# Kernel tuning notes

Measured on AMD Instinct MI355X. Metric: run time of the kernel, lower is better.

Reference implementation:

```python
import jax, jax.numpy as jnp
import numpy as np

N = 50000      # nodes
E = 1600000    # edges (avg degree 32)
D = 128        # feature dim (hardcoded by GATConv(128,128,1))
K = 3          # propagation order
NEG_SLOPE = 0.2  # DGL GATConv default leaky_relu slope


def setup_inputs() -> dict:
    key = jax.random.key(0)
    k1, k2, k3, k4, k5, k6, k7 = jax.random.split(key, 7)
    feats = jax.random.normal(k1, (N, D), dtype=jnp.float32)
    src = jax.random.randint(k2, (E,), 0, N, dtype=jnp.int32)
    dst = jax.random.randint(k3, (E,), 0, N, dtype=jnp.int32)
    W = jax.random.normal(k4, (D, D), dtype=jnp.float32) * 0.05
    attn_l = jax.random.normal(k5, (D,), dtype=jnp.float32) * 0.05
    attn_r = jax.random.normal(k6, (D,), dtype=jnp.float32) * 0.05
    bias = jax.random.normal(k7, (D,), dtype=jnp.float32) * 0.05
    return {"feats": feats, "W": W, "attn_l": attn_l, "attn_r": attn_r,
            "bias": bias, "src": src, "dst": dst}


def _grand_conv(feats, src, dst, order):
    seg = jax.ops.segment_sum
    ones = jnp.ones((src.shape[0],), feats.dtype)
    deg_in = jnp.maximum(seg(ones, dst, num_segments=N), 1.0)
    deg_out = jnp.maximum(seg(ones, src, num_segments=N), 1.0)
    norm1 = deg_in ** -0.5   # dst-side (in-degree) norm
    norm2 = deg_out ** -0.5  # src-side (out-degree) norm
    # rst = D_in^-1/2 A D_out^-1/2 feats  (one SpMM)
    nf = feats * norm2[:, None]
    rst = seg(nf[src], dst, num_segments=N) * norm1[:, None]
    # edge weight = norm1[src] * norm2[dst]  (fn.u_mul_v)
    w = (norm1[src] * norm2[dst])[:, None]  # [E,1]
    x = rst
    y = feats  # note: rst itself is NOT added (faithful to source)
    for _ in range(order):
        x = seg(x[src] * w, dst, num_segments=N)  # SpMM hop
        y = y + x
    return y / (order + 1)


def _gat(feat, W, attn_l, attn_r, bias, src, dst):
    seg = jax.ops.segment_sum
    h = feat @ W                      # [N,D]
    el = h @ attn_l                   # [N]
    er = h @ attn_r                   # [N]
    e = jax.nn.leaky_relu(el[src] + er[dst], NEG_SLOPE)  # [E]
    m = jax.ops.segment_max(e, dst, num_segments=N)      # stable edge-softmax
    a = jnp.exp(e - m[dst])
    s = seg(a, dst, num_segments=N)
    alpha = a / s[dst]
    out = seg(h[src] * alpha[:, None], dst, num_segments=N)
    return jax.nn.relu(out + bias)


def reference(feats, W, attn_l, attn_r, bias, src, dst):
    # drop_node with rate 0.0 is identity; S=1 so stacked mean is identity too.
    feat = _grand_conv(feats, src, dst, K)
    logits = _gat(feat, W, attn_l, attn_r, bias, src, dst)
    return jax.nn.log_softmax(logits, axis=-1)
```

## Files before the change

kernel.cpp:

```cpp
#include <hip/hip_runtime.h>
#include <hip/hip_bf16.h>
#include <math.h>

#define D 128
#define SB 512
#define GNUM 256
#define MAXW4 12512

typedef __attribute__((ext_vector_type(8))) short bf16x8;
typedef __attribute__((ext_vector_type(4))) float f32x4;
typedef __attribute__((ext_vector_type(2))) float fv2;

__device__ __forceinline__ bf16x8 pack8(const float* r) {
    union { bf16x8 v; __hip_bfloat162 h[4]; } u;
#pragma unroll
    for (int i = 0; i < 4; ++i)
        u.h[i] = __float22bfloat162_rn(make_float2(r[2 * i], r[2 * i + 1]));
    return u.v;
}

__device__ __forceinline__ uint2 packfp8x8(const float* r) {
    unsigned int w0 = 0, w1 = 0;
    w0 = __builtin_amdgcn_cvt_pk_fp8_f32(r[0], r[1], w0, false);
    w0 = __builtin_amdgcn_cvt_pk_fp8_f32(r[2], r[3], w0, true);
    w1 = __builtin_amdgcn_cvt_pk_fp8_f32(r[4], r[5], w1, false);
    w1 = __builtin_amdgcn_cvt_pk_fp8_f32(r[6], r[7], w1, true);
    return make_uint2(w0, w1);
}

__device__ __forceinline__ float fast_exp2(float x) {
#if __has_builtin(__builtin_amdgcn_exp2f)
    return __builtin_amdgcn_exp2f(x);
#else
    return exp2f(x);
#endif
}

__global__ __launch_bounds__(256) void histo_both(const int* __restrict__ src,
                                                  const int* __restrict__ dst,
                                                  unsigned int* __restrict__ Hs,
                                                  unsigned int* __restrict__ Hd,
                                                  int E, int N) {
    __shared__ unsigned int h[2 * MAXW4];
    int words = (N + 3) >> 2;
    for (int i = threadIdx.x; i < 2 * words; i += 256) h[i] = 0;
    __syncthreads();
    int per = (E + GNUM - 1) / GNUM;
    int lo = blockIdx.x * per;
    int hi = min(E, lo + per);
    for (int e = lo + (int)threadIdx.x; e < hi; e += 256) {
        int s = src[e];
        int d = dst[e];
        atomicAdd(&h[s >> 2], 1u << ((s & 3) * 8));
        atomicAdd(&h[words + (d >> 2)], 1u << ((d & 3) * 8));
    }
    __syncthreads();
    unsigned int* hsrow = Hs + (size_t)blockIdx.x * words;
    unsigned int* hdrow = Hd + (size_t)blockIdx.x * words;
    for (int i = threadIdx.x; i < words; i += 256) {
        hsrow[i] = h[i];
        hdrow[i] = h[words + i];
    }
}

__global__ void col_sum8(const unsigned char* __restrict__ H, float* __restrict__ n2, int N) {
    int bin = blockIdx.x * blockDim.x + threadIdx.x;
    if (bin >= N) return;
    size_t stride = (size_t)(((N + 3) >> 2) * 4);
    unsigned int s = 0;
    for (int b = 0; b < GNUM; ++b) s += H[(size_t)b * stride + bin];
    n2[bin] = rsqrtf((float)max((int)s, 1));
}

__global__ void col_scan8(unsigned char* __restrict__ Hd, int* __restrict__ deg_in,
                          float* __restrict__ n1, int N) {
    int bin = blockIdx.x * blockDim.x + threadIdx.x;
    if (bin >= N) return;
    size_t stride = (size_t)(((N + 3) >> 2) * 4);
    unsigned int run = 0;
    for (int b = 0; b < GNUM; ++b) {
        size_t o = (size_t)b * stride + bin;
        unsigned int hv = Hd[o];
        Hd[o] = (unsigned char)run;
        run += hv;
    }
    deg_in[bin] = (int)run;
    n1[bin] = rsqrtf((float)max((int)run, 1));
}

__global__ void scan_blocks(const int* __restrict__ in, int* __restrict__ out,
                            int* __restrict__ sums, int n) {
    __shared__ int sh[SB];
    int gid = blockIdx.x * SB + threadIdx.x;
    int v = (gid < n) ? in[gid] : 0;
    sh[threadIdx.x] = v;
    __syncthreads();
    for (int off = 1; off < SB; off <<= 1) {
        int t = (threadIdx.x >= off) ? sh[threadIdx.x - off] : 0;
        __syncthreads();
        sh[threadIdx.x] += t;
        __syncthreads();
    }
    if (gid < n) out[gid] = sh[threadIdx.x] - v;
    if (threadIdx.x == SB - 1) sums[blockIdx.x] = sh[threadIdx.x];
}

__global__ void scan_sums(int* sums, int nb) {
    __shared__ int sh[SB];
    int v = (threadIdx.x < nb) ? sums[threadIdx.x] : 0;
    sh[threadIdx.x] = v;
    __syncthreads();
    for (int off = 1; off < SB; off <<= 1) {
        int t = (threadIdx.x >= off) ? sh[threadIdx.x - off] : 0;
        __syncthreads();
        sh[threadIdx.x] += t;
        __syncthreads();
    }
    if (threadIdx.x < nb) sums[threadIdx.x] = sh[threadIdx.x] - v;
}

__global__ void scan_add(int* out, const int* __restrict__ sums, int n, int E) {
    int gid = blockIdx.x * SB + threadIdx.x;
    if (gid < n) out[gid] += sums[blockIdx.x];
    if (blockIdx.x == 0 && threadIdx.x == 0) out[n] = E;
}

__global__ __launch_bounds__(256) void fill_part(const int* __restrict__ src,
                                                 const int* __restrict__ dst,
                                                 const int* __restrict__ rowp,
                                                 const unsigned char* __restrict__ base,
                                                 int* __restrict__ csr, int E, int N) {
    __shared__ unsigned int cur[MAXW4];
    int words = (N + 3) >> 2;
    for (int i = threadIdx.x; i < words; i += 256) cur[i] = 0;
    __syncthreads();
    size_t stride = (size_t)(words * 4);
    int per = (E + GNUM - 1) / GNUM;
    int lo = blockIdx.x * per;
    int hi = min(E, lo + per);
    const unsigned char* brow = base + (size_t)blockIdx.x * stride;
    for (int e = lo + (int)threadIdx.x; e < hi; e += 256) {
        int d = dst[e];
        unsigned int sh = (d & 3) * 8;
        unsigned int r = atomicAdd(&cur[d >> 2], 1u << sh);
        int rank = (int)((r >> sh) & 0xFFu);
        int pos = rowp[d] + (int)brow[d] + rank;
        csr[pos] = src[e];
    }
}

__global__ void convert_nf8(const float* __restrict__ feats, const float* __restrict__ n2,
                            unsigned int* __restrict__ nf8, int N) {
    int t = blockIdx.x * blockDim.x + threadIdx.x;
    int n = t >> 5, l = t & 31;
    if (n >= N) return;
    float w = n2[n];
    float4 f = *reinterpret_cast<const float4*>(feats + (size_t)n * D + l * 4);
    unsigned int w0 = 0;
    w0 = __builtin_amdgcn_cvt_pk_fp8_f32(f.x * w, f.y * w, w0, false);
    w0 = __builtin_amdgcn_cvt_pk_fp8_f32(f.z * w, f.w * w, w0, true);
    nf8[(size_t)n * 32 + l] = w0;
}

__global__ void convert_W(const float* __restrict__ W, ushort* __restrict__ Wb) {
    int tid = blockIdx.x * blockDim.x + threadIdx.x;
    if (tid >= 2048) return;
    int c = tid >> 8, t = (tid >> 6) & 3, lane = tid & 63;
    int col = c * 16 + (lane & 15);
    int k0 = t * 32 + ((lane >> 4) << 3);
    ushort* outp = Wb + (size_t)tid * 8;
    for (int j = 0; j < 8; ++j) {
        __hip_bfloat16 b = __float2bfloat16(W[(size_t)(k0 + j) * D + col]);
        outp[j] = *reinterpret_cast<ushort*>(&b);
    }
}

template <int MODE>
__global__ __launch_bounds__(256) void spmm4(const uint2* __restrict__ xs8,
                                             const ushort* __restrict__ ypin,
                                             const float* __restrict__ feats,
                                             const int* __restrict__ rowp,
                                             const int* __restrict__ csr,
                                             const float* __restrict__ n1,
                                             const float* __restrict__ n2,
                                             ushort* __restrict__ yp,
                                             uint2* __restrict__ outs8, int N) {
    int lane = threadIdx.x & 63;
    int g = lane >> 4, c = lane & 15;
    int wid = ((blockIdx.x * blockDim.x + threadIdx.x) >> 6) * 4 + g;
    if (wid >= N) return;
    int beg = rowp[wid], end = rowp[wid + 1];
    fv2 acc2[4] = {{0.f, 0.f}, {0.f, 0.f}, {0.f, 0.f}, {0.f, 0.f}};
    for (int base = beg; base < end; base += 8) {
        int rem = end - base;
        int kn = rem < 8 ? rem : 8;
        int s_c = csr[base + min(c & 7, rem - 1)];
        uint2 v[8];
#pragma unroll
        for (int k = 0; k < 8; ++k) {
            int sk = __shfl(s_c, k, 16);
            if (k < kn) v[k] = xs8[(size_t)sk * 16 + c];
        }
#pragma unroll
        for (int k = 0; k < 8; ++k)
            if (k < kn) {
                acc2[0] += __builtin_amdgcn_cvt_pk_f32_fp8(v[k].x, false);
                acc2[1] += __builtin_amdgcn_cvt_pk_f32_fp8(v[k].x, true);
                acc2[2] += __builtin_amdgcn_cvt_pk_f32_fp8(v[k].y, false);
                acc2[3] += __builtin_amdgcn_cvt_pk_f32_fp8(v[k].y, true);
            }
    }
    float acc[8];
#pragma unroll
    for (int j = 0; j < 4; ++j) {
        acc[2 * j] = acc2[j][0];
        acc[2 * j + 1] = acc2[j][1];
    }
    if (MODE == 0) {
        float s1 = n1[wid];
        float sc = s1 * s1;
        float r[8];
#pragma unroll
        for (int i = 0; i < 8; ++i) r[i] = acc[i] * sc;
        outs8[(size_t)wid * 16 + c] = packfp8x8(r);
    } else if (MODE == 1 || MODE == 2) {
        float sp = n2[wid];
        float ss = sp * n1[wid];
        float xv[8], rs[8];
#pragma unroll
        for (int i = 0; i < 8; ++i) { xv[i] = acc[i] * sp; rs[i] = acc[i] * ss; }
        if (MODE == 2) {
            bf16x8 prev = *reinterpret_cast<const bf16x8*>(ypin + (size_t)wid * 128 + c * 8);
            const __hip_bfloat162* h2 = reinterpret_cast<const __hip_bfloat162*>(&prev);
#pragma unroll
            for (int i = 0; i < 4; ++i) {
                float2 v = __bfloat1622float2(h2[i]);
                xv[2 * i] += v.x;
                xv[2 * i + 1] += v.y;
            }
        }
        *reinterpret_cast<bf16x8*>(yp + (size_t)wid * 128 + c * 8) = pack8(xv);
        outs8[(size_t)wid * 16 + c] = packfp8x8(rs);
    } else {
        float sp = n2[wid];
        float4 f0 = *reinterpret_cast<const float4*>(feats + (size_t)wid * D + c * 8);
        float4 f1 = *reinterpret_cast<const float4*>(feats + (size_t)wid * D + c * 8 + 4);
        float ft[8] = {f0.x, f0.y, f0.z, f0.w, f1.x, f1.y, f1.z, f1.w};
        bf16x8 prev = *reinterpret_cast<const bf16x8*>(ypin + (size_t)wid * 128 + c * 8);
        const __hip_bfloat162* h2 = reinterpret_cast<const __hip_bfloat162*>(&prev);
        float r[8];
#pragma unroll
        for (int i = 0; i < 4; ++i) {
            float2 v = __bfloat1622float2(h2[i]);
            r[2 * i]     = 0.25f * (ft[2 * i] + v.x + acc[2 * i] * sp);
            r[2 * i + 1] = 0.25f * (ft[2 * i + 1] + v.y + acc[2 * i + 1] * sp);
        }
        *reinterpret_cast<bf16x8*>(yp + (size_t)wid * 128 + c * 8) = pack8(r);
    }
}

__global__ __launch_bounds__(256) void gat4(const uint2* __restrict__ h8,
                                            const int* __restrict__ rowp,
                                            const int* __restrict__ csr,
                                            const float2* __restrict__ elsc,
                                            const float* __restrict__ er,
                                            const float* __restrict__ bias,
                                            float* __restrict__ out, int N) {
    int lane = threadIdx.x & 63;
    int g = lane >> 4, c = lane & 15;
    int wid = ((blockIdx.x * blockDim.x + threadIdx.x) >> 6) * 4 + g;
    if (wid >= N) return;
    int beg = rowp[wid], end = rowp[wid + 1];
    float ern = er[wid];
    float ssum = 0.f;
    fv2 acc2[4] = {{0.f, 0.f}, {0.f, 0.f}, {0.f, 0.f}, {0.f, 0.f}};
    for (int base = beg; base < end; base += 8) {
        int rem = end - base;
        int kn = rem < 8 ? rem : 8;
        int s_c = csr[base + min(c & 7, rem - 1)];
        uint2 v[8];
        float2 es[8];
#pragma unroll
        for (int k = 0; k < 8; ++k) {
            int sk = __shfl(s_c, k, 16);
            if (k < kn) {
                v[k] = h8[(size_t)sk * 16 + c];
                es[k] = elsc[sk];
            }
        }
#pragma unroll
        for (int k = 0; k < 8; ++k)
            if (k < kn) {
                float t = es[k].x + ern;
                t = fmaxf(t, 0.2f * t);
                float p = fast_exp2(t);
                ssum += p;
                float w = p * es[k].y;
                fv2 wv = {w, w};
                acc2[0] += wv * __builtin_amdgcn_cvt_pk_f32_fp8(v[k].x, false);
                acc2[1] += wv * __builtin_amdgcn_cvt_pk_f32_fp8(v[k].x, true);
                acc2[2] += wv * __builtin_amdgcn_cvt_pk_f32_fp8(v[k].y, false);
                acc2[3] += wv * __builtin_amdgcn_cvt_pk_f32_fp8(v[k].y, true);
            }
    }
    float inv = ssum > 0.f ? 1.f / ssum : 0.f;
    float z[8];
    float mx = -INFINITY;
#pragma unroll
    for (int i = 0; i < 8; ++i) {
        z[i] = fmaxf(acc2[i >> 1][i & 1] * inv + bias[16 * i + c], 0.f);
        mx = fmaxf(mx, z[i]);
    }
#pragma unroll
    for (int off = 1; off < 16; off <<= 1) mx = fmaxf(mx, __shfl_xor(mx, off));
    float pz = 0.f;
#pragma unroll
    for (int i = 0; i < 8; ++i) pz += __expf(z[i] - mx);
#pragma unroll
    for (int off = 1; off < 16; off <<= 1) pz += __shfl_xor(pz, off);
    float ls = logf(pz);
    float* op = out + (size_t)wid * D;
#pragma unroll
    for (int i = 0; i < 8; ++i) op[16 * i + c] = z[i] - mx - ls;
}

__global__ __launch_bounds__(256) void gemm_mfma(const ushort* __restrict__ ybf,
                                                 const ushort* __restrict__ Wb,
                                                 const float* __restrict__ attnl,
                                                 const float* __restrict__ attnr,
                                                 unsigned char* __restrict__ h8,
                                                 float2* __restrict__ elsc,
                                                 float* __restrict__ er, int N) {
    __shared__ ushort Ws[16384];
    {
        const float4* srcv = reinterpret_cast<const float4*>(Wb);
        float4* dstv = reinterpret_cast<float4*>(Ws);
        for (int i = threadIdx.x; i < 2048; i += 256) dstv[i] = srcv[i];
    }
    __syncthreads();
    int wave = threadIdx.x >> 6, lane = threadIdx.x & 63;
    int base = blockIdx.x * 64 + wave * 16;
    if (base >= N) return;
    int col16 = lane & 15, rgrp = lane >> 4;

    int arow = base + col16;
    const bf16x8* yrow = reinterpret_cast<const bf16x8*>(ybf + (size_t)arow * 128);
    bf16x8 afrag[4];
#pragma unroll
    for (int t = 0; t < 4; ++t) afrag[t] = yrow[t * 4 + rgrp];

    const bf16x8* WsV = reinterpret_cast<const bf16x8*>(Ws);
    f32x4 acc[8];
#pragma unroll
    for (int c = 0; c < 8; ++c) acc[c] = (f32x4){0.f, 0.f, 0.f, 0.f};
#pragma unroll
    for (int c = 0; c < 8; ++c) {
#pragma unroll
        for (int t = 0; t < 4; ++t) {
            bf16x8 b = WsV[(c * 4 + t) * 64 + lane];
            acc[c] = __builtin_amdgcn_mfma_f32_16x16x32_bf16(afrag[t], b, acc[c], 0, 0, 0);
        }
    }

    float pl[4] = {0.f, 0.f, 0.f, 0.f}, pr[4] = {0.f, 0.f, 0.f, 0.f};
#pragma unroll
    for (int c = 0; c < 8; ++c) {
        float alc = attnl[c * 16 + col16];
        float arc = attnr[c * 16 + col16];
#pragma unroll
        for (int r = 0; r < 4; ++r) {
            pl[r] += acc[c][r] * alc;
            pr[r] += acc[c][r] * arc;
        }
    }
#pragma unroll
    for (int r = 0; r < 4; ++r) {
#pragma unroll
        for (int off = 8; off; off >>= 1) {
            pl[r] += __shfl_xor(pl[r], off);
            pr[r] += __shfl_xor(pr[r], off);
        }
    }

    float rmax[4];
#pragma unroll
    for (int r = 0; r < 4; ++r) {
        float m = 0.f;
#pragma unroll
        for (int c = 0; c < 8; ++c) m = fmaxf(m, fabsf(acc[c][r]));
#pragma unroll
        for (int off = 1; off < 16; off <<= 1) m = fmaxf(m, __shfl_xor(m, off));
        rmax[r] = fmaxf(m, 1e-20f);
    }

#pragma unroll
    for (int r = 0; r < 4; ++r) {
        float iv = 448.f / rmax[r];
        float rr[8];
#pragma unroll
        for (int c = 0; c < 8; ++c) rr[c] = acc[c][r] * iv;
        uint2 pk = packfp8x8(rr);
        int row = base + rgrp * 4 + r;
        *reinterpret_cast<uint2*>(h8 + (size_t)row * 128 + col16 * 8) = pk;
    }

    const float LOG2E = 1.44269504088896340736f;
    if (col16 == 0) {
#pragma unroll
        for (int r = 0; r < 4; ++r) {
            int row = base + rgrp * 4 + r;
            elsc[row] = make_float2(pl[r] * LOG2E, rmax[r] * (1.f / 448.f));
            er[row] = pr[r] * LOG2E;
        }
    }
}

extern "C" void kernel_launch(void* const* d_in, const int* in_sizes, int n_in,
                              void* d_out, int out_size, void* d_ws, size_t ws_size,
                              hipStream_t stream) {
    const float* feats  = (const float*)d_in[0];
    const float* W      = (const float*)d_in[1];
    const float* attn_l = (const float*)d_in[2];
    const float* attn_r = (const float*)d_in[3];
    const float* bias   = (const float*)d_in[4];
    const int*   src    = (const int*)d_in[5];
    const int*   dst    = (const int*)d_in[6];
    int N = in_sizes[0] / D;
    int E = in_sizes[5];
    float* out = (float*)d_out;

    char* p = (char*)d_ws;
    auto alloc = [&](size_t bytes) {
        char* r = p;
        p += (bytes + 255) & ~size_t(255);
        return r;
    };
    int*    deg_in = (int*)alloc((size_t)N * 4);
    int*    rowp   = (int*)alloc(((size_t)N + 1) * 4);
    int*    bsums  = (int*)alloc((size_t)SB * 4);
    float*  n1     = (float*)alloc((size_t)N * 4);
    float*  n2     = (float*)alloc((size_t)N * 4);
    float*  er     = (float*)alloc((size_t)N * 4);
    float2* elsc   = (float2*)alloc((size_t)N * 8);
    int*    csr    = (int*)alloc((size_t)E * 4);
    ushort* Wb     = (ushort*)alloc((size_t)16384 * 2);
    ushort* bufY1  = (ushort*)alloc((size_t)N * 128 * 2);
    ushort* bufY   = (ushort*)alloc((size_t)N * 128 * 2);
    uint2*  t0     = (uint2*)alloc((size_t)N * 16 * 8);
    uint2*  t1     = (uint2*)alloc((size_t)N * 16 * 8);
    uint2*  t2     = (uint2*)alloc((size_t)N * 16 * 8);
    unsigned int* Hs = (unsigned int*)bufY1;
    unsigned int* Hd = (unsigned int*)bufY;

    const int tb = 256;
    histo_both<<<GNUM, tb, 0, stream>>>(src, dst, Hs, Hd, E, N);
    col_sum8<<<(N + tb - 1) / tb, tb, 0, stream>>>((const unsigned char*)Hs, n2, N);
    col_scan8<<<(N + tb - 1) / tb, tb, 0, stream>>>((unsigned char*)Hd, deg_in, n1, N);
    int nb = (N + SB - 1) / SB;
    scan_blocks<<<nb, SB, 0, stream>>>(deg_in, rowp, bsums, N);
    scan_sums<<<1, SB, 0, stream>>>(bsums, nb);
    scan_add<<<nb, SB, 0, stream>>>(rowp, bsums, N, E);
    fill_part<<<GNUM, tb, 0, stream>>>(src, dst, rowp, (const unsigned char*)Hd, csr, E, N);
    convert_W<<<8, tb, 0, stream>>>(W, Wb);
    convert_nf8<<<((size_t)N * 32 + tb - 1) / tb, tb, 0, stream>>>(feats, n2,
                                                                   (unsigned int*)t1, N);

    int wgrid4 = (N + 15) / 16;
    spmm4<0><<<wgrid4, 256, 0, stream>>>(t1, nullptr, nullptr, rowp, csr, n1, n2,
                                         nullptr, t0, N);
    spmm4<1><<<wgrid4, 256, 0, stream>>>(t0, nullptr, nullptr, rowp, csr, n1, n2,
                                         bufY1, t1, N);
    spmm4<2><<<wgrid4, 256, 0, stream>>>(t1, bufY1, nullptr, rowp, csr, n1, n2,
                                         bufY1, t2, N);
    spmm4<3><<<wgrid4, 256, 0, stream>>>(t2, bufY1, feats, rowp, csr, n1, n2,
                                         bufY, nullptr, N);

    gemm_mfma<<<(N + 63) / 64, 256, 0, stream>>>(bufY, Wb, attn_l, attn_r,
                                                 (unsigned char*)t0, elsc, er, N);
    gat4<<<wgrid4, 256, 0, stream>>>((const uint2*)t0, rowp, csr, elsc, er, bias, out, N);
}
```

Baseline: 264.5 us.

## Use 8-lane 16-byte gathers per row in SpMM and GAT kernels

```diff
diff --git a/kernel.cpp b/kernel.cpp
--- a/kernel.cpp
+++ b/kernel.cpp
@@ -26,6 +26,51 @@
     w1 = __builtin_amdgcn_cvt_pk_fp8_f32(r[4], r[5], w1, false);
     w1 = __builtin_amdgcn_cvt_pk_fp8_f32(r[6], r[7], w1, true);
     return make_uint2(w0, w1);
+}
+
+__device__ __forceinline__ uint4 packfp8x16(const float* r) {
+    uint4 o;
+    unsigned int w;
+    w = 0;
+    w = __builtin_amdgcn_cvt_pk_fp8_f32(r[0], r[1], w, false);
+    w = __builtin_amdgcn_cvt_pk_fp8_f32(r[2], r[3], w, true);
+    o.x = w;
+    w = 0;
+    w = __builtin_amdgcn_cvt_pk_fp8_f32(r[4], r[5], w, false);
+    w = __builtin_amdgcn_cvt_pk_fp8_f32(r[6], r[7], w, true);
+    o.y = w;
+    w = 0;
+    w = __builtin_amdgcn_cvt_pk_fp8_f32(r[8], r[9], w, false);
+    w = __builtin_amdgcn_cvt_pk_fp8_f32(r[10], r[11], w, true);
+    o.z = w;
+    w = 0;
+    w = __builtin_amdgcn_cvt_pk_fp8_f32(r[12], r[13], w, false);
+    w = __builtin_amdgcn_cvt_pk_fp8_f32(r[14], r[15], w, true);
+    o.w = w;
+    return o;
+}
+
+__device__ __forceinline__ void acc_fp8x16(uint4 v, fv2* a) {
+    a[0] += __builtin_amdgcn_cvt_pk_f32_fp8(v.x, false);
+    a[1] += __builtin_amdgcn_cvt_pk_f32_fp8(v.x, true);
+    a[2] += __builtin_amdgcn_cvt_pk_f32_fp8(v.y, false);
+    a[3] += __builtin_amdgcn_cvt_pk_f32_fp8(v.y, true);
+    a[4] += __builtin_amdgcn_cvt_pk_f32_fp8(v.z, false);
+    a[5] += __builtin_amdgcn_cvt_pk_f32_fp8(v.z, true);
+    a[6] += __builtin_amdgcn_cvt_pk_f32_fp8(v.w, false);
+    a[7] += __builtin_amdgcn_cvt_pk_f32_fp8(v.w, true);
+}
+
+__device__ __forceinline__ void acc_fp8x16w(uint4 v, float w, fv2* a) {
+    fv2 wv = {w, w};
+    a[0] += wv * __builtin_amdgcn_cvt_pk_f32_fp8(v.x, false);
+    a[1] += wv * __builtin_amdgcn_cvt_pk_f32_fp8(v.x, true);
+    a[2] += wv * __builtin_amdgcn_cvt_pk_f32_fp8(v.y, false);
+    a[3] += wv * __builtin_amdgcn_cvt_pk_f32_fp8(v.y, true);
+    a[4] += wv * __builtin_amdgcn_cvt_pk_f32_fp8(v.z, false);
+    a[5] += wv * __builtin_amdgcn_cvt_pk_f32_fp8(v.z, true);
+    a[6] += wv * __builtin_amdgcn_cvt_pk_f32_fp8(v.w, false);
+    a[7] += wv * __builtin_amdgcn_cvt_pk_f32_fp8(v.w, true);
 }
 
 __device__ __forceinline__ float fast_exp2(float x) {
@@ -176,7 +221,7 @@
 }
 
 template <int MODE>
-__global__ __launch_bounds__(256) void spmm4(const uint2* __restrict__ xs8,
+__global__ __launch_bounds__(256) void spmmw(const uint4* __restrict__ xs16,
                                              const ushort* __restrict__ ypin,
                                              const float* __restrict__ feats,
                                              const int* __restrict__ rowp,
@@ -184,82 +229,98 @@
                                              const float* __restrict__ n1,
                                              const float* __restrict__ n2,
                                              ushort* __restrict__ yp,
-                                             uint2* __restrict__ outs8, int N) {
+                                             uint4* __restrict__ outs16, int N) {
     int lane = threadIdx.x & 63;
-    int g = lane >> 4, c = lane & 15;
-    int wid = ((blockIdx.x * blockDim.x + threadIdx.x) >> 6) * 4 + g;
+    int g = lane >> 3, c = lane & 7;
+    int wid = ((blockIdx.x * blockDim.x + threadIdx.x) >> 6) * 8 + g;
     if (wid >= N) return;
     int beg = rowp[wid], end = rowp[wid + 1];
-    fv2 acc2[4] = {{0.f, 0.f}, {0.f, 0.f}, {0.f, 0.f}, {0.f, 0.f}};
-    for (int base = beg; base < end; base += 8) {
-        int rem = end - base;
-        int kn = rem < 8 ? rem : 8;
-        int s_c = csr[base + min(c & 7, rem - 1)];
-        uint2 v[8];
+    fv2 acc2[8] = {{0.f, 0.f}, {0.f, 0.f}, {0.f, 0.f}, {0.f, 0.f},
+                   {0.f, 0.f}, {0.f, 0.f}, {0.f, 0.f}, {0.f, 0.f}};
+    int base = beg;
+    int cur_s = (beg < end) ? csr[beg + min(c, end - beg - 1)] : 0;
+    while (base < end) {
+        int nb = base + 8;
+        int next_s = 0;
+        if (nb < end) next_s = csr[nb + min(c, end - nb - 1)];
+        int kn = min(8, end - base);
+        uint4 v[8];
 #pragma unroll
         for (int k = 0; k < 8; ++k) {
-            int sk = __shfl(s_c, k, 16);
-            if (k < kn) v[k] = xs8[(size_t)sk * 16 + c];
+            int sk = __shfl(cur_s, k, 8);
+            if (k < kn) v[k] = xs16[(size_t)sk * 8 + c];
         }
 #pragma unroll
         for (int k = 0; k < 8; ++k)
-            if (k < kn) {
-                acc2[0] += __builtin_amdgcn_cvt_pk_f32_fp8(v[k].x, false);
-                acc2[1] += __builtin_amdgcn_cvt_pk_f32_fp8(v[k].x, true);
-                acc2[2] += __builtin_amdgcn_cvt_pk_f32_fp8(v[k].y, false);
-                acc2[3] += __builtin_amdgcn_cvt_pk_f32_fp8(v[k].y, true);
-            }
-    }
-    float acc[8];
-#pragma unroll
-    for (int j = 0; j < 4; ++j) {
+            if (k < kn) acc_fp8x16(v[k], acc2);
+        cur_s = next_s;
+        base = nb;
+    }
+    float acc[16];
+#pragma unroll
+    for (int j = 0; j < 8; ++j) {
         acc[2 * j] = acc2[j][0];
         acc[2 * j + 1] = acc2[j][1];
     }
     if (MODE == 0) {
         float s1 = n1[wid];
         float sc = s1 * s1;
-        float r[8];
-#pragma unroll
-        for (int i = 0; i < 8; ++i) r[i] = acc[i] * sc;
-        outs8[(size_t)wid * 16 + c] = packfp8x8(r);
+        float r[16];
+#pragma unroll
+        for (int i = 0; i < 16; ++i) r[i] = acc[i] * sc;
+        outs16[(size_t)wid * 8 + c] = packfp8x16(r);
     } else if (MODE == 1 || MODE == 2) {
         float sp = n2[wid];
         float ss = sp * n1[wid];
-        float xv[8], rs[8];
-#pragma unroll
-        for (int i = 0; i < 8; ++i) { xv[i] = acc[i] * sp; rs[i] = acc[i] * ss; }
+        float xv[16], rs[16];
+#pragma unroll
+        for (int i = 0; i < 16; ++i) { xv[i] = acc[i] * sp; rs[i] = acc[i] * ss; }
         if (MODE == 2) {
-            bf16x8 prev = *reinterpret_cast<const bf16x8*>(ypin + (size_t)wid * 128 + c * 8);
-            const __hip_bfloat162* h2 = reinterpret_cast<const __hip_bfloat162*>(&prev);
-#pragma unroll
-            for (int i = 0; i < 4; ++i) {
-                float2 v = __bfloat1622float2(h2[i]);
-                xv[2 * i] += v.x;
-                xv[2 * i + 1] += v.y;
+            const bf16x8* pv = reinterpret_cast<const bf16x8*>(ypin + (size_t)wid * 128 + c * 16);
+#pragma unroll
+            for (int hb = 0; hb < 2; ++hb) {
+                bf16x8 prev = pv[hb];
+                const __hip_bfloat162* h2 = reinterpret_cast<const __hip_bfloat162*>(&prev);
+#pragma unroll
+                for (int i = 0; i < 4; ++i) {
+                    float2 v2 = __bfloat1622float2(h2[i]);
+                    xv[8 * hb + 2 * i] += v2.x;
+                    xv[8 * hb + 2 * i + 1] += v2.y;
+                }
             }
         }
-        *reinterpret_cast<bf16x8*>(yp + (size_t)wid * 128 + c * 8) = pack8(xv);
-        outs8[(size_t)wid * 16 + c] = packfp8x8(rs);
+        bf16x8* ov = reinterpret_cast<bf16x8*>(yp + (size_t)wid * 128 + c * 16);
+        ov[0] = pack8(xv);
+        ov[1] = pack8(xv + 8);
+        outs16[(size_t)wid * 8 + c] = packfp8x16(rs);
     } else {
         float sp = n2[wid];
-        float4 f0 = *reinterpret_cast<const float4*>(feats + (size_t)wid * D + c * 8);
-        float4 f1 = *reinterpret_cast<const float4*>(feats + (size_t)wid * D + c * 8 + 4);
-        float ft[8] = {f0.x, f0.y, f0.z, f0.w, f1.x, f1.y, f1.z, f1.w};
-        bf16x8 prev = *reinterpret_cast<const bf16x8*>(ypin + (size_t)wid * 128 + c * 8);
-        const __hip_bfloat162* h2 = reinterpret_cast<const __hip_bfloat162*>(&prev);
-        float r[8];
-#pragma unroll
-        for (int i = 0; i < 4; ++i) {
-            float2 v = __bfloat1622float2(h2[i]);
-            r[2 * i]     = 0.25f * (ft[2 * i] + v.x + acc[2 * i] * sp);
-            r[2 * i + 1] = 0.25f * (ft[2 * i + 1] + v.y + acc[2 * i + 1] * sp);
-        }
-        *reinterpret_cast<bf16x8*>(yp + (size_t)wid * 128 + c * 8) = pack8(r);
-    }
-}
-
-__global__ __launch_bounds__(256) void gat4(const uint2* __restrict__ h8,
+        float ft[16];
+#pragma unroll
+        for (int q4 = 0; q4 < 4; ++q4) {
+            float4 f = *reinterpret_cast<const float4*>(feats + (size_t)wid * D + c * 16 + q4 * 4);
+            ft[4 * q4] = f.x; ft[4 * q4 + 1] = f.y; ft[4 * q4 + 2] = f.z; ft[4 * q4 + 3] = f.w;
+        }
+        float r[16];
+        const bf16x8* pv = reinterpret_cast<const bf16x8*>(ypin + (size_t)wid * 128 + c * 16);
+#pragma unroll
+        for (int hb = 0; hb < 2; ++hb) {
+            bf16x8 prev = pv[hb];
+            const __hip_bfloat162* h2 = reinterpret_cast<const __hip_bfloat162*>(&prev);
+#pragma unroll
+            for (int i = 0; i < 4; ++i) {
+                float2 v2 = __bfloat1622float2(h2[i]);
+                r[8 * hb + 2 * i]     = 0.25f * (ft[8 * hb + 2 * i] + v2.x + acc[8 * hb + 2 * i] * sp);
+                r[8 * hb + 2 * i + 1] = 0.25f * (ft[8 * hb + 2 * i + 1] + v2.y + acc[8 * hb + 2 * i + 1] * sp);
+            }
+        }
+        bf16x8* ov = reinterpret_cast<bf16x8*>(yp + (size_t)wid * 128 + c * 16);
+        ov[0] = pack8(r);
+        ov[1] = pack8(r + 8);
+    }
+}
+
+__global__ __launch_bounds__(256) void gatw(const uint4* __restrict__ h16,
                                             const int* __restrict__ rowp,
                                             const int* __restrict__ csr,
                                             const float2* __restrict__ elsc,
@@ -267,61 +328,71 @@
                                             const float* __restrict__ bias,
                                             float* __restrict__ out, int N) {
     int lane = threadIdx.x & 63;
-    int g = lane >> 4, c = lane & 15;
-    int wid = ((blockIdx.x * blockDim.x + threadIdx.x) >> 6) * 4 + g;
+    int g = lane >> 3, c = lane & 7;
+    int wid = ((blockIdx.x * blockDim.x + threadIdx.x) >> 6) * 8 + g;
     if (wid >= N) return;
     int beg = rowp[wid], end = rowp[wid + 1];
     float ern = er[wid];
-    float ssum = 0.f;
-    fv2 acc2[4] = {{0.f, 0.f}, {0.f, 0.f}, {0.f, 0.f}, {0.f, 0.f}};
-    for (int base = beg; base < end; base += 8) {
-        int rem = end - base;
-        int kn = rem < 8 ? rem : 8;
-        int s_c = csr[base + min(c & 7, rem - 1)];
-        uint2 v[8];
-        float2 es[8];
+    float psum = 0.f;
+    fv2 acc2[8] = {{0.f, 0.f}, {0.f, 0.f}, {0.f, 0.f}, {0.f, 0.f},
+                   {0.f, 0.f}, {0.f, 0.f}, {0.f, 0.f}, {0.f, 0.f}};
+    int base = beg;
+    int cur_s = (beg < end) ? csr[beg + min(c, end - beg - 1)] : 0;
+    while (base < end) {
+        int nb = base + 8;
+        int next_s = 0;
+        if (nb < end) next_s = csr[nb + min(c, end - nb - 1)];
+        int kn = min(8, end - base);
+        float2 es = elsc[cur_s];
+        float t = es.x + ern;
+        t = fmaxf(t, 0.2f * t);
+        float p = (c < kn) ? fast_exp2(t) : 0.f;
+        psum += p;
+        float wv = p * es.y;
+        uint4 v[8];
 #pragma unroll
         for (int k = 0; k < 8; ++k) {
-            int sk = __shfl(s_c, k, 16);
-            if (k < kn) {
-                v[k] = h8[(size_t)sk * 16 + c];
-                es[k] = elsc[sk];
-            }
+            int sk = __shfl(cur_s, k, 8);
+            if (k < kn) v[k] = h16[(size_t)sk * 8 + c];
         }
 #pragma unroll
         for (int k = 0; k < 8; ++k)
             if (k < kn) {
-                float t = es[k].x + ern;
-                t = fmaxf(t, 0.2f * t);
-                float p = fast_exp2(t);
-                ssum += p;
-                float w = p * es[k].y;
-                fv2 wv = {w, w};
-                acc2[0] += wv * __builtin_amdgcn_cvt_pk_f32_fp8(v[k].x, false);
-                acc2[1] += wv * __builtin_amdgcn_cvt_pk_f32_fp8(v[k].x, true);
-                acc2[2] += wv * __builtin_amdgcn_cvt_pk_f32_fp8(v[k].y, false);
-                acc2[3] += wv * __builtin_amdgcn_cvt_pk_f32_fp8(v[k].y, true);
+                float wk = __shfl(wv, k, 8);
+                acc_fp8x16w(v[k], wk, acc2);
             }
-    }
-    float inv = ssum > 0.f ? 1.f / ssum : 0.f;
-    float z[8];
+        cur_s = next_s;
+        base = nb;
+    }
+    psum += __shfl_xor(psum, 1, 8);
+    psum += __shfl_xor(psum, 2, 8);
+    psum += __shfl_xor(psum, 4, 8);
+    float inv = psum > 0.f ? 1.f / psum : 0.f;
+    float zA[8], zB[8];
     float mx = -INFINITY;
 #pragma unroll
-    for (int i = 0; i < 8; ++i) {
-        z[i] = fmaxf(acc2[i >> 1][i & 1] * inv + bias[16 * i + c], 0.f);
-        mx = fmaxf(mx, z[i]);
-    }
-#pragma unroll
-    for (int off = 1; off < 16; off <<= 1) mx = fmaxf(mx, __shfl_xor(mx, off));
+    for (int j = 0; j < 8; ++j) {
+        float2 b2 = *reinterpret_cast<const float2*>(bias + 16 * j + 2 * c);
+        zA[j] = fmaxf(acc2[j >> 1][j & 1] * inv + b2.x, 0.f);
+        zB[j] = fmaxf(acc2[(j + 8) >> 1][(j + 8) & 1] * inv + b2.y, 0.f);
+        mx = fmaxf(mx, fmaxf(zA[j], zB[j]));
+    }
+    mx = fmaxf(mx, __shfl_xor(mx, 1, 8));
+    mx = fmaxf(mx, __shfl_xor(mx, 2, 8));
+    mx = fmaxf(mx, __shfl_xor(mx, 4, 8));
     float pz = 0.f;
 #pragma unroll
-    for (int i = 0; i < 8; ++i) pz += __expf(z[i] - mx);
-#pragma unroll
-    for (int off = 1; off < 16; off <<= 1) pz += __shfl_xor(pz, off);
+    for (int j = 0; j < 8; ++j) pz += __expf(zA[j] - mx) + __expf(zB[j] - mx);
+    pz += __shfl_xor(pz, 1, 8);
+    pz += __shfl_xor(pz, 2, 8);
+    pz += __shfl_xor(pz, 4, 8);
     float ls = logf(pz);
     float* op = out + (size_t)wid * D;
 #pragma unroll
-    for (int i = 0; i < 8; ++i) op[16 * i + c] = z[i] - mx - ls;
+    for (int j = 0; j < 8; ++j) {
+        float2 o2 = make_float2(zA[j] - mx - ls, zB[j] - mx - ls);
+        *reinterpret_cast<float2*>(op + 16 * j + 2 * c) = o2;
+    }
 }
 
 __global__ __launch_bounds__(256) void gemm_mfma(const ushort* __restrict__ ybf,
@@ -446,9 +517,9 @@
     ushort* Wb     = (ushort*)alloc((size_t)16384 * 2);
     ushort* bufY1  = (ushort*)alloc((size_t)N * 128 * 2);
     ushort* bufY   = (ushort*)alloc((size_t)N * 128 * 2);
-    uint2*  t0     = (uint2*)alloc((size_t)N * 16 * 8);
-    uint2*  t1     = (uint2*)alloc((size_t)N * 16 * 8);
-    uint2*  t2     = (uint2*)alloc((size_t)N * 16 * 8);
+    uint4*  t0     = (uint4*)alloc((size_t)N * 8 * 16);
+    uint4*  t1     = (uint4*)alloc((size_t)N * 8 * 16);
+    uint4*  t2     = (uint4*)alloc((size_t)N * 8 * 16);
     unsigned int* Hs = (unsigned int*)bufY1;
     unsigned int* Hd = (unsigned int*)bufY;
 
@@ -465,17 +536,17 @@
     convert_nf8<<<((size_t)N * 32 + tb - 1) / tb, tb, 0, stream>>>(feats, n2,
                                                                    (unsigned int*)t1, N);
 
-    int wgrid4 = (N + 15) / 16;
-    spmm4<0><<<wgrid4, 256, 0, stream>>>(t1, nullptr, nullptr, rowp, csr, n1, n2,
+    int wgrid8 = (N + 31) / 32;
+    spmmw<0><<<wgrid8, 256, 0, stream>>>(t1, nullptr, nullptr, rowp, csr, n1, n2,
                                          nullptr, t0, N);
-    spmm4<1><<<wgrid4, 256, 0, stream>>>(t0, nullptr, nullptr, rowp, csr, n1, n2,
+    spmmw<1><<<wgrid8, 256, 0, stream>>>(t0, nullptr, nullptr, rowp, csr, n1, n2,
                                          bufY1, t1, N);
-    spmm4<2><<<wgrid4, 256, 0, stream>>>(t1, bufY1, nullptr, rowp, csr, n1, n2,
+    spmmw<2><<<wgrid8, 256, 0, stream>>>(t1, bufY1, nullptr, rowp, csr, n1, n2,
                                          bufY1, t2, N);
-    spmm4<3><<<wgrid4, 256, 0, stream>>>(t2, bufY1, feats, rowp, csr, n1, n2,
+    spmmw<3><<<wgrid8, 256, 0, stream>>>(t2, bufY1, feats, rowp, csr, n1, n2,
                                          bufY, nullptr, N);
 
     gemm_mfma<<<(N + 63) / 64, 256, 0, stream>>>(bufY, Wb, attn_l, attn_r,
                                                  (unsigned char*)t0, elsc, er, N);
-    gat4<<<wgrid4, 256, 0, stream>>>((const uint2*)t0, rowp, csr, elsc, er, bias, out, N);
-}
+    gatw<<<wgrid8, 256, 0, stream>>>((const uint4*)t0, rowp, csr, elsc, er, bias, out, N);
+}
```

Result: no change. 263.2 us (-0.5%).
